# Optimization experiments

Measured on AMD Instinct MI355X. Metric: run time of the kernel, lower is better.

Reference implementation:

```python
import jax, jax.numpy as jnp
import numpy as np

# Ground-plane grid from proj_2DTo2D: W = 640/4 = 160, H = 480/4 = 120
GP_H, GP_W = 120, 160
PATCH_NUM = 1


def setup_inputs() -> dict:
    key = jax.random.key(0)
    k1, k2, k3 = jax.random.split(key, 3)
    nR, fh, fw, fdim = 4, 90, 160, 512  # 4 camera views, quarter-res feature maps
    nV = GP_H * GP_W  # 19200 ground-plane points per view
    inputs = jax.random.normal(k1, (nR, fh, fw, fdim), dtype=jnp.float32)
    # Projected image-plane coordinates (stand-in for calibration-based World2Image)
    im_x = jax.random.uniform(k2, (nR, nV), dtype=jnp.float32) * (fw - 1)
    im_y = jax.random.uniform(k3, (nR, nV), dtype=jnp.float32) * (fh - 1)
    return {"inputs": inputs, "im_x": im_x, "im_y": im_y}


def reference(inputs, im_x, im_y):
    # inputs: [nR, fh, fw, fdim]; im_x/im_y: [nR, nV] float pixel coords
    nR, fh, fw, fdim = inputs.shape
    im_x = jnp.clip(im_x, 0.0, fw - 1)
    im_y = jnp.clip(im_y, 0.0, fh - 1)
    x0 = jnp.floor(im_x).astype(jnp.int32)
    x1 = jnp.clip(x0 + 1, 0, fw - 1)
    y0 = jnp.floor(im_y).astype(jnp.int32)
    y1 = jnp.clip(y0 + 1, 0, fh - 1)
    x0f, x1f = x0.astype(im_x.dtype), x1.astype(im_x.dtype)
    y0f, y1f = y0.astype(im_y.dtype), y1.astype(im_y.dtype)

    b = jnp.arange(nR)[:, None]  # [nR, 1] batch index per grid point
    Ia = inputs[b, y0, x0]  # [nR, nV, fdim]
    Ib = inputs[b, y1, x0]
    Ic = inputs[b, y0, x1]
    Id = inputs[b, y1, x1]

    wa = ((x1f - im_x) * (y1f - im_y))[..., None]
    wb = ((x1f - im_x) * (im_y - y0f))[..., None]
    wc = ((im_x - x0f) * (y1f - im_y))[..., None]
    wd = ((im_x - x0f) * (im_y - y0f))[..., None]

    Ibilin = wa * Ia + wb * Ib + wc * Ic + wd * Id  # [nR, nV, fdim]
    return Ibilin.reshape(nR // PATCH_NUM, PATCH_NUM, GP_H, GP_W, fdim)
```

## Files before the change

kernel.cpp:

```cpp
#include <hip/hip_runtime.h>


typedef float f32x4 __attribute__((ext_vector_type(4)));

constexpr int NR   = 4;
constexpr int FH   = 90;
constexpr int FW   = 160;
constexpr int FDIM = 512;
constexpr int NV   = 120 * 160;
constexpr int NPTS = NR * NV;
constexpr int C4   = FDIM / 4;

constexpr int BY   = 3;
constexpr int BX   = 5;
constexpr int NGY  = FH / BY;
constexpr int NGX  = FW / BX;
constexpr int NBINS = NR * NGY * NGX;
constexpr int SY   = BY + 1;
constexpr int SX   = BX + 1;
constexpr int SCELLS = SY * SX;

constexpr int CAP   = 48;
constexpr int OVCAP = 4096;

__global__ void k_zero(int* __restrict__ cnts) {
    int i = blockIdx.x * blockDim.x + threadIdx.x;
    if (i < NBINS + 1) cnts[i] = 0;
}

__global__ void k_scatter(const float* __restrict__ imx, const float* __restrict__ imy,
                          int* __restrict__ binCnt, int* __restrict__ ovCnt,
                          int* __restrict__ perm, float* __restrict__ sX,
                          float* __restrict__ sY, int* __restrict__ ovList) {
    int pt = blockIdx.x * blockDim.x + threadIdx.x;
    if (pt >= NPTS) return;
    int r = pt / NV;
    float x = imx[pt], y = imy[pt];
    x = fminf(fmaxf(x, 0.0f), (float)(FW - 1));
    y = fminf(fmaxf(y, 0.0f), (float)(FH - 1));
    int x0 = (int)floorf(x);
    int y0 = (int)floorf(y);
    int b = (r * NGY + y0 / BY) * NGX + x0 / BX;
    int slot = atomicAdd(&binCnt[b], 1);
    if (slot < CAP) {
        int idx = b * CAP + slot;
        perm[idx] = pt;
        sX[idx] = x;
        sY[idx] = y;
    } else {
        int o = atomicAdd(ovCnt, 1);
        if (o < OVCAP) ovList[o] = pt;
    }
}

__device__ __forceinline__ f32x4 lerp4(f32x4 A, f32x4 B, f32x4 C, f32x4 D,
                                       float wa, float wb, float wc, float wd) {
    return wa * A + wb * B + wc * C + wd * D;
}

__device__ __forceinline__ void weights_and_cells(float x, float y,
                                                  int& x0, int& x1, int& y0, int& y1,
                                                  float& wa, float& wb, float& wc, float& wd) {
    float x0f = floorf(x), y0f = floorf(y);
    x0 = (int)x0f; y0 = (int)y0f;
    x1 = min(x0 + 1, FW - 1);
    y1 = min(y0 + 1, FH - 1);
    float wx1 = (float)x1 - x;
    float wx0 = x - x0f;
    float wy1 = (float)y1 - y;
    float wy0 = y - y0f;
    wa = wx1 * wy1; wb = wx1 * wy0; wc = wx0 * wy1; wd = wx0 * wy0;
}

__global__ __launch_bounds__(256) void st_bins(
    const float* __restrict__ inp,
    const int* __restrict__ binCnt,
    const int* __restrict__ ovCnt,
    const int* __restrict__ perm,
    const float* __restrict__ sX,
    const float* __restrict__ sY,
    const int* __restrict__ ovList,
    const float* __restrict__ imx,
    const float* __restrict__ imy,
    float* __restrict__ out)
{
    __shared__ f32x4 lds[SCELLS * C4];

    int p = blockIdx.x;
    int b = (p & 7) * (NBINS >> 3) + (p >> 3);

    int r   = b / (NGY * NGX);
    int by0 = (b / NGX % NGY) * BY;
    int bx0 = (b % NGX) * BX;
    int tid = threadIdx.x;

    const f32x4* in4 = (const f32x4*)inp;
    #pragma unroll
    for (int i = 0; i < (SCELLS * C4) / 256; ++i) {
        int idx  = tid + i * 256;
        int cell = idx >> 7;
        int c4   = idx & (C4 - 1);
        int ry   = cell / SX;
        int rx   = cell - ry * SX;
        int gy   = min(by0 + ry, FH - 1);
        int gx   = min(bx0 + rx, FW - 1);
        lds[idx] = in4[(size_t)((r * FH + gy) * FW + gx) * C4 + c4];
    }

    int cnt  = min(binCnt[b], CAP);
    int base = b * CAP;
    __syncthreads();

    int half = tid >> 7;
    int c4   = tid & (C4 - 1);
    f32x4* out4 = (f32x4*)out;

    int i = half;
    for (; i + 2 < cnt; i += 4) {
        int   ptA = perm[base + i];
        float xA  = sX[base + i], yA = sY[base + i];
        int   ptB = perm[base + i + 2];
        float xB  = sX[base + i + 2], yB = sY[base + i + 2];

        int x0A, x1A, y0A, y1A, x0B, x1B, y0B, y1B;
        float waA, wbA, wcA, wdA, waB, wbB, wcB, wdB;
        weights_and_cells(xA, yA, x0A, x1A, y0A, y1A, waA, wbA, wcA, wdA);
        weights_and_cells(xB, yB, x0B, x1B, y0B, y1B, waB, wbB, wcB, wdB);

        f32x4 Aa = lds[(((y0A - by0) * SX + (x0A - bx0)) << 7) + c4];
        f32x4 Ab = lds[(((y1A - by0) * SX + (x0A - bx0)) << 7) + c4];
        f32x4 Ac = lds[(((y0A - by0) * SX + (x1A - bx0)) << 7) + c4];
        f32x4 Ad = lds[(((y1A - by0) * SX + (x1A - bx0)) << 7) + c4];
        f32x4 Ba = lds[(((y0B - by0) * SX + (x0B - bx0)) << 7) + c4];
        f32x4 Bb = lds[(((y1B - by0) * SX + (x0B - bx0)) << 7) + c4];
        f32x4 Bc = lds[(((y0B - by0) * SX + (x1B - bx0)) << 7) + c4];
        f32x4 Bd = lds[(((y1B - by0) * SX + (x1B - bx0)) << 7) + c4];

        __builtin_nontemporal_store(lerp4(Aa, Ab, Ac, Ad, waA, wbA, wcA, wdA),
                                    out4 + (size_t)ptA * C4 + c4);
        __builtin_nontemporal_store(lerp4(Ba, Bb, Bc, Bd, waB, wbB, wcB, wdB),
                                    out4 + (size_t)ptB * C4 + c4);
    }
    if (i < cnt) {
        int   pt = perm[base + i];
        float x  = sX[base + i], y = sY[base + i];
        int x0, x1, y0, y1; float wa, wb, wc, wd;
        weights_and_cells(x, y, x0, x1, y0, y1, wa, wb, wc, wd);
        f32x4 A = lds[(((y0 - by0) * SX + (x0 - bx0)) << 7) + c4];
        f32x4 B = lds[(((y1 - by0) * SX + (x0 - bx0)) << 7) + c4];
        f32x4 C = lds[(((y0 - by0) * SX + (x1 - bx0)) << 7) + c4];
        f32x4 D = lds[(((y1 - by0) * SX + (x1 - bx0)) << 7) + c4];
        __builtin_nontemporal_store(lerp4(A, B, C, D, wa, wb, wc, wd),
                                    out4 + (size_t)pt * C4 + c4);
    }

    int ov = min(*ovCnt, OVCAP);
    for (int j = b; j < ov; j += NBINS) {
        if (half != 0) continue;
        int pt = ovList[j];
        int rr = pt / NV;
        float x = imx[pt], y = imy[pt];
        x = fminf(fmaxf(x, 0.0f), (float)(FW - 1));
        y = fminf(fmaxf(y, 0.0f), (float)(FH - 1));
        int x0, x1, y0, y1; float wa, wb, wc, wd;
        weights_and_cells(x, y, x0, x1, y0, y1, wa, wb, wc, wd);
        int rb = rr * FH;
        f32x4 A = in4[(size_t)((rb + y0) * FW + x0) * C4 + c4];
        f32x4 B = in4[(size_t)((rb + y1) * FW + x0) * C4 + c4];
        f32x4 C = in4[(size_t)((rb + y0) * FW + x1) * C4 + c4];
        f32x4 D = in4[(size_t)((rb + y1) * FW + x1) * C4 + c4];
        __builtin_nontemporal_store(lerp4(A, B, C, D, wa, wb, wc, wd),
                                    out4 + (size_t)pt * C4 + c4);
    }
}

__global__ __launch_bounds__(256) void st_bilinear_direct(
    const float* __restrict__ inp,
    const float* __restrict__ imx,
    const float* __restrict__ imy,
    float* __restrict__ out)
{
    int gid = blockIdx.x * blockDim.x + threadIdx.x;
    int pt = gid >> 7;
    int c4 = gid & (C4 - 1);
    if (pt >= NPTS) return;
    int r = pt / NV;
    float x = imx[pt], y = imy[pt];
    x = fminf(fmaxf(x, 0.0f), (float)(FW - 1));
    y = fminf(fmaxf(y, 0.0f), (float)(FH - 1));
    int x0, x1, y0, y1; float wa, wb, wc, wd;
    weights_and_cells(x, y, x0, x1, y0, y1, wa, wb, wc, wd);
    const f32x4* base = (const f32x4*)inp;
    int rb = r * FH;
    f32x4 a = base[(size_t)((rb + y0) * FW + x0) * C4 + c4];
    f32x4 b = base[(size_t)((rb + y1) * FW + x0) * C4 + c4];
    f32x4 c = base[(size_t)((rb + y0) * FW + x1) * C4 + c4];
    f32x4 d = base[(size_t)((rb + y1) * FW + x1) * C4 + c4];
    ((f32x4*)out)[(size_t)pt * C4 + c4] = lerp4(a, b, c, d, wa, wb, wc, wd);
}

extern "C" void kernel_launch(void* const* d_in, const int* in_sizes, int n_in,
                              void* d_out, int out_size, void* d_ws, size_t ws_size,
                              hipStream_t stream) {
    const float* inp = (const float*)d_in[0];
    const float* imx = (const float*)d_in[1];
    const float* imy = (const float*)d_in[2];
    float* out = (float*)d_out;

    size_t nInts = (size_t)NBINS + 1 + (size_t)NBINS * CAP * 3 + OVCAP;
    size_t need  = nInts * sizeof(int);

    if (ws_size < need) {
        int nblocks = (NPTS * C4) / 256;
        hipLaunchKernelGGL(st_bilinear_direct, dim3(nblocks), dim3(256), 0, stream,
                           inp, imx, imy, out);
        return;
    }

    int*   binCnt = (int*)d_ws;
    int*   ovCnt  = binCnt + NBINS;
    int*   perm   = ovCnt + 1;
    float* sX     = (float*)(perm + NBINS * CAP);
    float* sY     = sX + NBINS * CAP;
    int*   ovList = (int*)(sY + NBINS * CAP);

    hipLaunchKernelGGL(k_zero, dim3((NBINS + 1 + 255) / 256), dim3(256), 0, stream,
                       binCnt);
    hipLaunchKernelGGL(k_scatter, dim3((NPTS + 255) / 256), dim3(256), 0, stream,
                       imx, imy, binCnt, ovCnt, perm, sX, sY, ovList);
    hipLaunchKernelGGL(st_bins, dim3(NBINS), dim3(256), 0, stream,
                       inp, binCnt, ovCnt, perm, sX, sY, ovList, imx, imy, out);
}
```

Before: 60.69 us.

## Use direct global-to-LDS loads, stage bin metadata in LDS, double block size

```diff
diff --git a/kernel.cpp b/kernel.cpp
--- a/kernel.cpp
+++ b/kernel.cpp
@@ -2,6 +2,9 @@
 
 
 typedef float f32x4 __attribute__((ext_vector_type(4)));
+
+#define GLOBAL_AS __attribute__((address_space(1)))
+#define LDS_AS    __attribute__((address_space(3)))
 
 constexpr int NR   = 4;
 constexpr int FH   = 90;
@@ -22,6 +25,7 @@
 
 constexpr int CAP   = 48;
 constexpr int OVCAP = 4096;
+constexpr int TPB   = 512;
 
 __global__ void k_zero(int* __restrict__ cnts) {
     int i = blockIdx.x * blockDim.x + threadIdx.x;
@@ -72,7 +76,7 @@
     wa = wx1 * wy1; wb = wx1 * wy0; wc = wx0 * wy1; wd = wx0 * wy0;
 }
 
-__global__ __launch_bounds__(256) void st_bins(
+__global__ __launch_bounds__(TPB) void st_bins(
     const float* __restrict__ inp,
     const int* __restrict__ binCnt,
     const int* __restrict__ ovCnt,
@@ -85,6 +89,9 @@
     float* __restrict__ out)
 {
     __shared__ f32x4 lds[SCELLS * C4];
+    __shared__ int   pmS[CAP];
+    __shared__ float pxS[CAP];
+    __shared__ float pyS[CAP];
 
     int p = blockIdx.x;
     int b = (p & 7) * (NBINS >> 3) + (p >> 3);
@@ -95,32 +102,40 @@
     int tid = threadIdx.x;
 
     const f32x4* in4 = (const f32x4*)inp;
+    int cnt  = min(binCnt[b], CAP);
+    int base = b * CAP;
+
     #pragma unroll
-    for (int i = 0; i < (SCELLS * C4) / 256; ++i) {
-        int idx  = tid + i * 256;
+    for (int i = 0; i < (SCELLS * C4) / TPB; ++i) {
+        int idx  = tid + i * TPB;
         int cell = idx >> 7;
         int c4   = idx & (C4 - 1);
         int ry   = cell / SX;
         int rx   = cell - ry * SX;
         int gy   = min(by0 + ry, FH - 1);
         int gx   = min(bx0 + rx, FW - 1);
-        lds[idx] = in4[(size_t)((r * FH + gy) * FW + gx) * C4 + c4];
-    }
-
-    int cnt  = min(binCnt[b], CAP);
-    int base = b * CAP;
+        const void* gsrc = (const void*)(in4 + (size_t)((r * FH + gy) * FW + gx) * C4 + c4);
+        __builtin_amdgcn_global_load_lds(
+            (const GLOBAL_AS void*)gsrc,
+            (LDS_AS void*)&lds[idx], 16, 0, 0);
+    }
+    if (tid < cnt) {
+        pmS[tid] = perm[base + tid];
+        pxS[tid] = sX[base + tid];
+        pyS[tid] = sY[base + tid];
+    }
     __syncthreads();
 
-    int half = tid >> 7;
-    int c4   = tid & (C4 - 1);
+    int g  = tid >> 7;
+    int c4 = tid & (C4 - 1);
     f32x4* out4 = (f32x4*)out;
 
-    int i = half;
-    for (; i + 2 < cnt; i += 4) {
-        int   ptA = perm[base + i];
-        float xA  = sX[base + i], yA = sY[base + i];
-        int   ptB = perm[base + i + 2];
-        float xB  = sX[base + i + 2], yB = sY[base + i + 2];
+    int i = g;
+    for (; i + 4 < cnt; i += 8) {
+        int   ptA = pmS[i];
+        float xA  = pxS[i], yA = pyS[i];
+        int   ptB = pmS[i + 4];
+        float xB  = pxS[i + 4], yB = pyS[i + 4];
 
         int x0A, x1A, y0A, y1A, x0B, x1B, y0B, y1B;
         float waA, wbA, wcA, wdA, waB, wbB, wcB, wdB;
@@ -142,8 +157,8 @@
                                     out4 + (size_t)ptB * C4 + c4);
     }
     if (i < cnt) {
-        int   pt = perm[base + i];
-        float x  = sX[base + i], y = sY[base + i];
+        int   pt = pmS[i];
+        float x  = pxS[i], y = pyS[i];
         int x0, x1, y0, y1; float wa, wb, wc, wd;
         weights_and_cells(x, y, x0, x1, y0, y1, wa, wb, wc, wd);
         f32x4 A = lds[(((y0 - by0) * SX + (x0 - bx0)) << 7) + c4];
@@ -156,7 +171,7 @@
 
     int ov = min(*ovCnt, OVCAP);
     for (int j = b; j < ov; j += NBINS) {
-        if (half != 0) continue;
+        if (g != 0) continue;
         int pt = ovList[j];
         int rr = pt / NV;
         float x = imx[pt], y = imy[pt];
@@ -228,6 +243,6 @@
                        binCnt);
     hipLaunchKernelGGL(k_scatter, dim3((NPTS + 255) / 256), dim3(256), 0, stream,
                        imx, imy, binCnt, ovCnt, perm, sX, sY, ovList);
-    hipLaunchKernelGGL(st_bins, dim3(NBINS), dim3(256), 0, stream,
+    hipLaunchKernelGGL(st_bins, dim3(NBINS), dim3(TPB), 0, stream,
                        inp, binCnt, ovCnt, perm, sX, sY, ovList, imx, imy, out);
 }
```

New measurement: 58.87 us. 1.03x faster.
